# Performance work log

Hardware: AMD Instinct MI355X
Metric: run time of the kernel (lower is better)

## Reference

```python
import jax, jax.numpy as jnp
import numpy as np

N, E = 100000, 640000
IN_DIM, OUT_DIM, H, D = 128, 128, 4, 32  # head_dim = out_dim // num_heads
NUM_EDGE_TYPES = 3
NEG_SLOPE = 0.2


def setup_inputs() -> dict:
    key = jax.random.key(0)
    ks = jax.random.split(key, 10)
    x = jax.random.normal(ks[0], (N, IN_DIM), dtype=jnp.float32)
    edge_index = jax.random.randint(ks[1], (2, E), 0, N, dtype=jnp.int32)
    edge_type = jax.random.randint(ks[2], (E,), 0, NUM_EDGE_TYPES, dtype=jnp.int32)
    s = 1.0 / np.sqrt(IN_DIM)
    Wq = jax.random.uniform(ks[3], (IN_DIM, H * D), jnp.float32, -s, s)
    Wk = jax.random.uniform(ks[4], (IN_DIM, H * D), jnp.float32, -s, s)
    Wv = jax.random.uniform(ks[5], (IN_DIM, H * D), jnp.float32, -s, s)
    # xavier_uniform on (1, H, 2D): gain*sqrt(6/(fan_in+fan_out)) with fans (2D, H)
    a = np.sqrt(6.0 / (2 * D + H))
    attn_lin = jax.random.uniform(ks[6], (1, H, 2 * D), jnp.float32, -a, a)
    edge_embed_table = jax.random.normal(ks[7], (NUM_EDGE_TYPES, H * D), dtype=jnp.float32)
    so = 1.0 / np.sqrt(H * D)
    Wout = jax.random.uniform(ks[8], (H * D, OUT_DIM), jnp.float32, -so, so)
    bout = jax.random.uniform(ks[9], (OUT_DIM,), jnp.float32, -so, so)
    return {"x": x, "Wq": Wq, "Wk": Wk, "Wv": Wv, "attn_lin": attn_lin,
            "edge_embed_table": edge_embed_table, "Wout": Wout, "bout": bout,
            "edge_index": edge_index, "edge_type": edge_type}


def reference(x, Wq, Wk, Wv, attn_lin, edge_embed_table, Wout, bout, edge_index, edge_type):
    n = x.shape[0]
    src, dst = edge_index[0], edge_index[1]
    q = (x @ Wq).reshape(n, H, D)
    k = (x @ Wk).reshape(n, H, D)
    v = (x @ Wv).reshape(n, H, D)
    q_src = q[src]            # (E, H, D)
    k_dst = k[dst]            # (E, H, D)
    # (cat([q_src,k_dst]) * attn_lin).sum(-1) == q_src.a_q + k_dst.a_k
    a_q, a_k = attn_lin[0, :, :D], attn_lin[0, :, D:]      # (H, D) each
    scores = jnp.einsum('ehd,hd->eh', q_src, a_q) + jnp.einsum('ehd,hd->eh', k_dst, a_k)
    scores = jnp.where(scores >= 0, scores, NEG_SLOPE * scores)  # leaky_relu
    edge_embed = edge_embed_table[edge_type].reshape(-1, H, D)
    scores = scores + jnp.sum(q_src * edge_embed, axis=-1)       # (E, H)
    # segmented softmax over destination node (detached max, clamped at -100)
    m = jax.ops.segment_max(jax.lax.stop_gradient(scores), dst, num_segments=n)
    m = jnp.maximum(m, -100.0)
    ex = jnp.exp(scores - m[dst])
    denom = jax.ops.segment_sum(ex, dst, num_segments=n)
    alpha = ex / (denom[dst] + 1e-10)                            # (E, H)
    messages = alpha[:, :, None] * v[src]                        # (E, H, D)
    out = jax.ops.segment_sum(messages, dst, num_segments=n)     # (N, H, D)
    out = out.reshape(n, H * D)
    return out @ Wout + bout
```

## Files before the change

### kernel.cpp

```cpp
#include <hip/hip_runtime.h>
#include <hip/hip_bf16.h>

#define H_   4
#define D_   32
#define HD   128
#define IND  128
#define OUTD 128
#define NET  3
#define NEG  0.2f
#define CAP  2048

typedef short short8 __attribute__((ext_vector_type(8)));
typedef float f32x4  __attribute__((ext_vector_type(4)));

#define AS_GLOBAL(p) ((const __attribute__((address_space(1))) unsigned int*)(p))
#define AS_LDS(p)    ((__attribute__((address_space(3))) unsigned int*)(p))

__device__ __forceinline__ unsigned short f2bf(float f) {
  union { __hip_bfloat16 b; unsigned short u; } x;
  x.b = __float2bfloat16(f);
  return x.u;
}

__device__ __forceinline__ short8 pack_bf8(float4 lo, float4 hi) {
  union { short8 s; unsigned short u[8]; } r;
  r.u[0] = f2bf(lo.x); r.u[1] = f2bf(lo.y); r.u[2] = f2bf(lo.z); r.u[3] = f2bf(lo.w);
  r.u[4] = f2bf(hi.x); r.u[5] = f2bf(hi.y); r.u[6] = f2bf(hi.z); r.u[7] = f2bf(hi.w);
  return r.s;
}

#define BFLO(x) __uint_as_float((x) << 16)
#define BFHI(x) __uint_as_float((x) & 0xFFFF0000u)

__global__ void k0b_pack(const float* __restrict__ Wq, const float* __restrict__ Wk,
                         const float* __restrict__ attn, const float* __restrict__ ee,
                         const float* __restrict__ Wv, const float* __restrict__ Wout,
                         unsigned short* __restrict__ Wallt,
                         unsigned short* __restrict__ Woutt,
                         int* __restrict__ gbuck, int nbuck) {
  int b = blockIdx.x, i = threadIdx.x;
  if (b == 288) {
    for (int k = i; k < nbuck; k += 128) gbuck[k] = 0;
    return;
  }
  if (b < 160) {
    int c = b;
    float val = 0.f;
    if (c < 128) {
      val = Wv[i*HD + c];
    } else {
      int cc = c - 128;
      if (cc < 4) {
        int h = cc;
        for (int d = 0; d < D_; d++) val += Wq[i*HD + h*D_ + d] * attn[h*2*D_ + d];
      } else if (cc < 16) {
        int t2 = (cc - 4) >> 2, h = (cc - 4) & 3;
        for (int d = 0; d < D_; d++) val += Wq[i*HD + h*D_ + d] * ee[t2*HD + h*D_ + d];
      } else if (cc < 20) {
        int h = cc - 16;
        for (int d = 0; d < D_; d++) val += Wk[i*HD + h*D_ + d] * attn[h*2*D_ + D_ + d];
      }
    }
    Wallt[(c*128 + i) ^ ((c & 7) << 3)] = f2bf(val);
  } else {
    int c = b - 160;
    Woutt[(c*128 + i) ^ ((c & 7) << 3)] = f2bf(Wout[i*OUTD + c]);
  }
}

__global__ __launch_bounds__(256) void k1b(const float* __restrict__ x,
    const uint4* __restrict__ Wallt,
    unsigned short* __restrict__ vb, unsigned short* __restrict__ nqb,
    float* __restrict__ skb, int n, int nbb,
    const int* __restrict__ ei, const int* __restrict__ et,
    int* __restrict__ gbuck, unsigned int* __restrict__ ebuf,
    int E_, int nbuck, int per) {
  extern __shared__ char dlds[];
  int t = threadIdx.x;
  if (blockIdx.x < nbb) {
    int* cnt  = (int*)dlds;
    int* base = cnt + 1024;
    for (int i = t; i < nbuck; i += 256) cnt[i] = 0;
    __syncthreads();
    int bb = blockIdx.x;
    int e0 = bb * per;
    int e1 = min(e0 + per, E_);
    for (int e = e0 + t; e < e1; e += 256)
      atomicAdd(&cnt[ei[E_ + e] >> 7], 1);
    __syncthreads();
    for (int i = t; i < nbuck; i += 256) {
      int c = cnt[i];
      base[i] = c ? atomicAdd(&gbuck[i], c) : 0;
      cnt[i] = 0;
    }
    __syncthreads();
    for (int e = e0 + t; e < e1; e += 256) {
      int d = ei[E_ + e];
      int b = d >> 7;
      int pos = base[b] + atomicAdd(&cnt[b], 1);
      ebuf[(size_t)b * CAP + pos] =
          (unsigned)ei[e] | ((unsigned)et[e] << 17) | ((unsigned)(d & 127) << 19);
    }
    return;
  }
  uint4* ldsB = (uint4*)dlds;
  int wv = t >> 6, lane = t & 63;
  int l15 = lane & 15, l16 = lane >> 4;
  int base = (blockIdx.x - nbb) * 64;
  int arow = base + wv*16 + l15;
  int rr = min(arow, n - 1);
  const float* xr = &x[(size_t)rr*IND + l16*8];
  float4 lo[4], hi[4];
  #pragma unroll
  for (int kk = 0; kk < 4; kk++) {
    lo[kk] = *(const float4*)(xr + kk*32);
    hi[kk] = *(const float4*)(xr + kk*32 + 4);
  }
  #pragma unroll
  for (int i = 0; i < 10; i++) {
    const uint4* gp = Wallt + i*256 + wv*64 + lane;
    uint4* lp = ldsB + i*256 + wv*64;
    __builtin_amdgcn_global_load_lds(AS_GLOBAL(gp), AS_LDS(lp), 16, 0, 0);
  }
  short8 afr[4];
  #pragma unroll
  for (int kk = 0; kk < 4; kk++) afr[kk] = pack_bf8(lo[kk], hi[kk]);
  __syncthreads();
  f32x4 acc[10];
  #pragma unroll
  for (int nt = 0; nt < 10; nt++) acc[nt] = (f32x4){0.f, 0.f, 0.f, 0.f};
  #pragma unroll
  for (int nt = 0; nt < 10; nt++) {
    int bcol = nt*16 + l15;
    #pragma unroll
    for (int kk = 0; kk < 4; kk++) {
      int bytec = kk*64 + l16*16;
      short8 b = *(const short8*)((const char*)ldsB + ((bcol*256 + bytec) ^ ((bcol & 7) << 4)));
      acc[nt] = __builtin_amdgcn_mfma_f32_16x16x32_bf16(afr[kk], b, acc[nt], 0, 0, 0);
    }
  }
  int rowbase = base + wv*16 + l16*4;
  #pragma unroll
  for (int nt = 0; nt < 10; nt++) {
    int col = nt*16 + l15;
    #pragma unroll
    for (int r = 0; r < 4; r++) {
      int row = rowbase + r;
      if (row >= n) continue;
      float val = acc[nt][r];
      if (nt < 8)       vb[(size_t)row*HD + col] = f2bf(val);
      else if (nt == 8) nqb[((size_t)row << 4) + (col - 128)] = f2bf(val);
      else { int c = col - 144; if (c < 4) skb[(size_t)row*4 + c] = val; }
    }
  }
}

__global__ __launch_bounds__(256) void k_sort(const unsigned int* __restrict__ ebuf,
    const int* __restrict__ gbuck, int* __restrict__ offsets,
    int* __restrict__ elist, int n, int E_) {
  __shared__ int cnt[128], cur[128], sc[128], red[256];
  int b = blockIdx.x, t = threadIdx.x;
  int part = 0;
  for (int i = t; i < b; i += 256) part += gbuck[i];
  red[t] = part; __syncthreads();
  for (int off = 128; off > 0; off >>= 1) {
    if (t < off) red[t] += red[t + off];
    __syncthreads();
  }
  int bb = red[0];
  int m = gbuck[b];
  if (b == 0 && t == 0) offsets[n] = E_;
  if (t < 128) cnt[t] = 0;
  __syncthreads();
  const unsigned int* eb = ebuf + (size_t)b * CAP;
  for (int i = t; i < m; i += 256)
    atomicAdd(&cnt[(eb[i] >> 19) & 127], 1);
  __syncthreads();
  if (t < 128) sc[t] = cnt[t];
  __syncthreads();
  for (int off = 1; off < 128; off <<= 1) {
    int v = (t >= off && t < 128) ? sc[t - off] : 0;
    __syncthreads();
    if (t < 128) sc[t] += v;
    __syncthreads();
  }
  if (t < 128) {
    int excl = sc[t] - cnt[t];
    cur[t] = excl;
    int dst = b * 128 + t;
    if (dst < n) offsets[dst] = bb + excl;
  }
  __syncthreads();
  for (int i = t; i < m; i += 256) {
    unsigned int w = eb[i];
    int dl = (w >> 19) & 127;
    int p = bb + atomicAdd(&cur[dl], 1);
    elist[p] = (int)((w & 0x1FFFFu) | (((w >> 17) & 3u) << 20));
  }
}

__global__ __launch_bounds__(256) void k3_agg(
    const int* __restrict__ offsets, const int* __restrict__ elist,
    const unsigned short* __restrict__ nqb, const float* __restrict__ skb,
    const unsigned short* __restrict__ vb, unsigned short* __restrict__ aggb, int n) {
  int t = threadIdx.x;
  int g = t >> 4, s = t & 15;
  int dst = blockIdx.x * 16 + g;
  __shared__ float s_esc[16][17][4];
  __shared__ int s_src[16][17];
  if (dst >= n) return;
  int off0 = offsets[dst];
  int deg = offsets[dst + 1] - off0;
  int h = s >> 2;
  unsigned short* orow = &aggb[(size_t)dst*HD + s*8];
  if (deg == 0) {
    *(uint4*)orow = make_uint4(0u, 0u, 0u, 0u);
    return;
  }
  float4 sk4 = *(const float4*)(&skb[(size_t)dst*4]);
  float dp0 = 0.f, dp1 = 0.f, dp2 = 0.f, dp3 = 0.f;
  float a0=0.f,a1=0.f,a2=0.f,a3=0.f,a4=0.f,a5=0.f,a6=0.f,a7=0.f;
  for (int bas = 0; bas < deg; bas += 16) {
    int cnt = min(16, deg - bas);
    float e0 = 0.f, e1 = 0.f, e2 = 0.f, e3 = 0.f;
    int srcoff = 0;
    if (s < cnt) {
      int p = elist[off0 + bas + s];
      int src = p & 0xFFFFF;
      int ety = p >> 20;
      const unsigned short* nr = nqb + ((size_t)src << 4);
      uint2 sqp = *(const uint2*)nr;
      uint2 qep = *(const uint2*)(nr + 4 + ety*4);
      float s0 = BFLO(sqp.x) + sk4.x;
      float s1 = BFHI(sqp.x) + sk4.y;
      float s2 = BFLO(sqp.y) + sk4.z;
      float s3 = BFHI(sqp.y) + sk4.w;
      s0 = (s0 >= 0.f ? s0 : NEG*s0) + BFLO(qep.x); e0 = __expf(s0);
      s1 = (s1 >= 0.f ? s1 : NEG*s1) + BFHI(qep.x); e1 = __expf(s1);
      s2 = (s2 >= 0.f ? s2 : NEG*s2) + BFLO(qep.y); e2 = __expf(s2);
      s3 = (s3 >= 0.f ? s3 : NEG*s3) + BFHI(qep.y); e3 = __expf(s3);
      dp0 += e0; dp1 += e1; dp2 += e2; dp3 += e3;
      srcoff = src << 7;
    }
    s_src[g][s] = srcoff;
    *(float4*)(&s_esc[g][s][0]) = make_float4(e0, e1, e2, e3);
    __builtin_amdgcn_wave_barrier();
    int e = 0;
    for (; e + 4 <= cnt; e += 4) {
      float al0 = s_esc[g][e+0][h], al1 = s_esc[g][e+1][h];
      float al2 = s_esc[g][e+2][h], al3 = s_esc[g][e+3][h];
      const unsigned short* p0 = vb + s_src[g][e+0] + s*8;
      const unsigned short* p1 = vb + s_src[g][e+1] + s*8;
      const unsigned short* p2 = vb + s_src[g][e+2] + s*8;
      const unsigned short* p3 = vb + s_src[g][e+3] + s*8;
      uint4 v0 = *(const uint4*)p0;
      uint4 v1 = *(const uint4*)p1;
      uint4 v2 = *(const uint4*)p2;
      uint4 v3 = *(const uint4*)p3;
      a0 += al0 * BFLO(v0.x); a1 += al0 * BFHI(v0.x);
      a2 += al0 * BFLO(v0.y); a3 += al0 * BFHI(v0.y);
      a4 += al0 * BFLO(v0.z); a5 += al0 * BFHI(v0.z);
      a6 += al0 * BFLO(v0.w); a7 += al0 * BFHI(v0.w);
      a0 += al1 * BFLO(v1.x); a1 += al1 * BFHI(v1.x);
      a2 += al1 * BFLO(v1.y); a3 += al1 * BFHI(v1.y);
      a4 += al1 * BFLO(v1.z); a5 += al1 * BFHI(v1.z);
      a6 += al1 * BFLO(v1.w); a7 += al1 * BFHI(v1.w);
      a0 += al2 * BFLO(v2.x); a1 += al2 * BFHI(v2.x);
      a2 += al2 * BFLO(v2.y); a3 += al2 * BFHI(v2.y);
      a4 += al2 * BFLO(v2.z); a5 += al2 * BFHI(v2.z);
      a6 += al2 * BFLO(v2.w); a7 += al2 * BFHI(v2.w);
      a0 += al3 * BFLO(v3.x); a1 += al3 * BFHI(v3.x);
      a2 += al3 * BFLO(v3.y); a3 += al3 * BFHI(v3.y);
      a4 += al3 * BFLO(v3.z); a5 += al3 * BFHI(v3.z);
      a6 += al3 * BFLO(v3.w); a7 += al3 * BFHI(v3.w);
    }
    for (; e < cnt; e++) {
      float a = s_esc[g][e][h];
      const unsigned short* p = vb + s_src[g][e] + s*8;
      uint4 vv = *(const uint4*)p;
      a0 += a * BFLO(vv.x); a1 += a * BFHI(vv.x);
      a2 += a * BFLO(vv.y); a3 += a * BFHI(vv.y);
      a4 += a * BFLO(vv.z); a5 += a * BFHI(vv.z);
      a6 += a * BFLO(vv.w); a7 += a * BFHI(vv.w);
    }
    __builtin_amdgcn_wave_barrier();
  }
  #pragma unroll
  for (int off = 1; off < 16; off <<= 1) {
    dp0 += __shfl_xor(dp0, off);
    dp1 += __shfl_xor(dp1, off);
    dp2 += __shfl_xor(dp2, off);
    dp3 += __shfl_xor(dp3, off);
  }
  float den = (h == 0) ? dp0 : (h == 1) ? dp1 : (h == 2) ? dp2 : dp3;
  float inv = 1.f / (den + 1e-10f);
  uint4 pk;
  pk.x = (unsigned)f2bf(a0*inv) | ((unsigned)f2bf(a1*inv) << 16);
  pk.y = (unsigned)f2bf(a2*inv) | ((unsigned)f2bf(a3*inv) << 16);
  pk.z = (unsigned)f2bf(a4*inv) | ((unsigned)f2bf(a5*inv) << 16);
  pk.w = (unsigned)f2bf(a6*inv) | ((unsigned)f2bf(a7*inv) << 16);
  *(uint4*)orow = pk;
}

__global__ __launch_bounds__(256) void k4_gemm(const unsigned short* __restrict__ aggb,
    const uint4* __restrict__ Woutt, const float* __restrict__ bout,
    float* __restrict__ out, int n) {
  __shared__ uint4 ldsB[2048];
  int t = threadIdx.x;
  #pragma unroll
  for (int i = 0; i < 8; i++) ldsB[i*256 + t] = Woutt[i*256 + t];
  int wv = t >> 6, lane = t & 63;
  int l15 = lane & 15, l16 = lane >> 4;
  int base = blockIdx.x * 64;
  int arow = base + wv*16 + l15;
  int rr = min(arow, n - 1);
  const unsigned short* ar = &aggb[(size_t)rr*HD + l16*8];
  short8 afr[4];
  #pragma unroll
  for (int kk = 0; kk < 4; kk++)
    afr[kk] = *(const short8*)(ar + kk*32);
  __syncthreads();
  f32x4 acc[8];
  #pragma unroll
  for (int nt = 0; nt < 8; nt++) acc[nt] = (f32x4){0.f, 0.f, 0.f, 0.f};
  #pragma unroll
  for (int nt = 0; nt < 8; nt++) {
    int bcol = nt*16 + l15;
    #pragma unroll
    for (int kk = 0; kk < 4; kk++) {
      int bytec = kk*64 + l16*16;
      short8 b = *(const short8*)((const char*)ldsB + ((bcol*256 + bytec) ^ ((bcol & 7) << 4)));
      acc[nt] = __builtin_amdgcn_mfma_f32_16x16x32_bf16(afr[kk], b, acc[nt], 0, 0, 0);
    }
  }
  int rowbase = base + wv*16 + l16*4;
  #pragma unroll
  for (int nt = 0; nt < 8; nt++) {
    int col = nt*16 + l15;
    float bv = bout[col];
    #pragma unroll
    for (int r = 0; r < 4; r++) {
      int row = rowbase + r;
      if (row < n) out[(size_t)row*OUTD + col] = acc[nt][r] + bv;
    }
  }
}

extern "C" void kernel_launch(void* const* d_in, const int* in_sizes, int n_in,
                              void* d_out, int out_size, void* d_ws, size_t ws_size,
                              hipStream_t stream) {
  const float* x    = (const float*)d_in[0];
  const float* Wq   = (const float*)d_in[1];
  const float* Wk   = (const float*)d_in[2];
  const float* Wv   = (const float*)d_in[3];
  const float* attn = (const float*)d_in[4];
  const float* ee   = (const float*)d_in[5];
  const float* Wout = (const float*)d_in[6];
  const float* bout = (const float*)d_in[7];
  const int*   ei   = (const int*)d_in[8];
  const int*   et   = (const int*)d_in[9];
  int n  = in_sizes[0] / IND;
  int E_ = in_sizes[9];
  float* out = (float*)d_out;
  int nbuck = (n + 127) >> 7;

  char* w = (char*)d_ws;
  auto alloc = [&](size_t bytes) {
    char* p = w;
    w += (bytes + 255) & ~(size_t)255;
    return p;
  };
  unsigned short* vb    = (unsigned short*)alloc((size_t)n * HD * 2);
  unsigned short* aggb  = (unsigned short*)alloc((size_t)n * HD * 2);
  unsigned short* nqb   = (unsigned short*)alloc((size_t)n * 16 * 2);
  float* skb      = (float*)alloc((size_t)n * 4 * 4);
  unsigned short* Wallt = (unsigned short*)alloc(160 * 128 * 2);
  unsigned short* Woutt = (unsigned short*)alloc(128 * 128 * 2);
  unsigned int* ebuf = (unsigned int*)alloc((size_t)nbuck * CAP * 4);
  int*   gbuck    = (int*)alloc((size_t)nbuck * 4);
  int*   offsets  = (int*)alloc(((size_t)n + 1) * 4);
  int*   elist    = (int*)alloc((size_t)E_ * 4);

  k0b_pack<<<289, 128, 0, stream>>>(Wq, Wk, attn, ee, Wv, Wout, Wallt, Woutt,
                                    gbuck, nbuck);
  int nblk1 = (n + 63) / 64;
  int nbb = 256;
  int per = (E_ + nbb - 1) / nbb;
  k1b<<<nbb + nblk1, 256, 40960, stream>>>(x, (const uint4*)Wallt, vb, nqb, skb,
                                           n, nbb, ei, et, gbuck, ebuf,
                                           E_, nbuck, per);
  k_sort<<<nbuck, 256, 0, stream>>>(ebuf, gbuck, offsets, elist, n, E_);
  k3_agg<<<(n + 15)/16, 256, 0, stream>>>(offsets, elist, nqb, skb, vb, aggb, n);
  k4_gemm<<<(n + 63)/64, 256, 0, stream>>>(aggb, (const uint4*)Woutt, bout, out, n);
}
```

Before: 98.18 us.

## Fuse per-bucket counting sort into aggregation kernel using LDS edge lists

Merges the bucket sort and the attention aggregation into one kernel. Each block sorts its 128-destination bucket into shared memory and then aggregates those destinations directly. This removes the global offsets/elist round trip, the prefix sum over buckets, and one launch. In exchange there are far fewer blocks (one per 128 nodes, about 782), each wave handles 8 destinations serially, and each block uses about 8KB+ of LDS, which may lower occupancy and latency hiding for the gather-heavy loop.

```diff
diff --git a/kernel.cpp b/kernel.cpp
--- a/kernel.cpp
+++ b/kernel.cpp
@@ -119,7 +119,7 @@
   #pragma unroll
   for (int i = 0; i < 10; i++) {
     const uint4* gp = Wallt + i*256 + wv*64 + lane;
-    uint4* lp = ldsB + i*256 + wv*64;
+    uint4* lp = (uint4*)dlds + i*256 + wv*64;
     __builtin_amdgcn_global_load_lds(AS_GLOBAL(gp), AS_LDS(lp), 16, 0, 0);
   }
   short8 afr[4];
@@ -155,21 +155,16 @@
   }
 }
 
-__global__ __launch_bounds__(256) void k_sort(const unsigned int* __restrict__ ebuf,
-    const int* __restrict__ gbuck, int* __restrict__ offsets,
-    int* __restrict__ elist, int n, int E_) {
-  __shared__ int cnt[128], cur[128], sc[128], red[256];
+__global__ __launch_bounds__(256) void k3f(const unsigned int* __restrict__ ebuf,
+    const int* __restrict__ gbuck,
+    const unsigned short* __restrict__ nqb, const float* __restrict__ skb,
+    const unsigned short* __restrict__ vb, unsigned short* __restrict__ aggb, int n) {
+  __shared__ unsigned int el[CAP];
+  __shared__ int cnt[128], cur[128], sc[128];
+  __shared__ float s_esc[16][17][4];
+  __shared__ int s_src[16][17];
   int b = blockIdx.x, t = threadIdx.x;
-  int part = 0;
-  for (int i = t; i < b; i += 256) part += gbuck[i];
-  red[t] = part; __syncthreads();
-  for (int off = 128; off > 0; off >>= 1) {
-    if (t < off) red[t] += red[t + off];
-    __syncthreads();
-  }
-  int bb = red[0];
   int m = gbuck[b];
-  if (b == 0 && t == 0) offsets[n] = E_;
   if (t < 128) cnt[t] = 0;
   __syncthreads();
   const unsigned int* eb = ebuf + (size_t)b * CAP;
@@ -184,122 +179,111 @@
     if (t < 128) sc[t] += v;
     __syncthreads();
   }
-  if (t < 128) {
-    int excl = sc[t] - cnt[t];
-    cur[t] = excl;
-    int dst = b * 128 + t;
-    if (dst < n) offsets[dst] = bb + excl;
-  }
+  if (t < 128) cur[t] = sc[t] - cnt[t];
   __syncthreads();
   for (int i = t; i < m; i += 256) {
     unsigned int w = eb[i];
     int dl = (w >> 19) & 127;
-    int p = bb + atomicAdd(&cur[dl], 1);
-    elist[p] = (int)((w & 0x1FFFFu) | (((w >> 17) & 3u) << 20));
-  }
-}
-
-__global__ __launch_bounds__(256) void k3_agg(
-    const int* __restrict__ offsets, const int* __restrict__ elist,
-    const unsigned short* __restrict__ nqb, const float* __restrict__ skb,
-    const unsigned short* __restrict__ vb, unsigned short* __restrict__ aggb, int n) {
-  int t = threadIdx.x;
+    el[atomicAdd(&cur[dl], 1)] = w;
+  }
+  __syncthreads();
   int g = t >> 4, s = t & 15;
-  int dst = blockIdx.x * 16 + g;
-  __shared__ float s_esc[16][17][4];
-  __shared__ int s_src[16][17];
-  if (dst >= n) return;
-  int off0 = offsets[dst];
-  int deg = offsets[dst + 1] - off0;
   int h = s >> 2;
-  unsigned short* orow = &aggb[(size_t)dst*HD + s*8];
-  if (deg == 0) {
-    *(uint4*)orow = make_uint4(0u, 0u, 0u, 0u);
-    return;
-  }
-  float4 sk4 = *(const float4*)(&skb[(size_t)dst*4]);
-  float dp0 = 0.f, dp1 = 0.f, dp2 = 0.f, dp3 = 0.f;
-  float a0=0.f,a1=0.f,a2=0.f,a3=0.f,a4=0.f,a5=0.f,a6=0.f,a7=0.f;
-  for (int bas = 0; bas < deg; bas += 16) {
-    int cnt = min(16, deg - bas);
-    float e0 = 0.f, e1 = 0.f, e2 = 0.f, e3 = 0.f;
-    int srcoff = 0;
-    if (s < cnt) {
-      int p = elist[off0 + bas + s];
-      int src = p & 0xFFFFF;
-      int ety = p >> 20;
-      const unsigned short* nr = nqb + ((size_t)src << 4);
-      uint2 sqp = *(const uint2*)nr;
-      uint2 qep = *(const uint2*)(nr + 4 + ety*4);
-      float s0 = BFLO(sqp.x) + sk4.x;
-      float s1 = BFHI(sqp.x) + sk4.y;
-      float s2 = BFLO(sqp.y) + sk4.z;
-      float s3 = BFHI(sqp.y) + sk4.w;
-      s0 = (s0 >= 0.f ? s0 : NEG*s0) + BFLO(qep.x); e0 = __expf(s0);
-      s1 = (s1 >= 0.f ? s1 : NEG*s1) + BFHI(qep.x); e1 = __expf(s1);
-      s2 = (s2 >= 0.f ? s2 : NEG*s2) + BFLO(qep.y); e2 = __expf(s2);
-      s3 = (s3 >= 0.f ? s3 : NEG*s3) + BFHI(qep.y); e3 = __expf(s3);
-      dp0 += e0; dp1 += e1; dp2 += e2; dp3 += e3;
-      srcoff = src << 7;
-    }
-    s_src[g][s] = srcoff;
-    *(float4*)(&s_esc[g][s][0]) = make_float4(e0, e1, e2, e3);
-    __builtin_amdgcn_wave_barrier();
-    int e = 0;
-    for (; e + 4 <= cnt; e += 4) {
-      float al0 = s_esc[g][e+0][h], al1 = s_esc[g][e+1][h];
-      float al2 = s_esc[g][e+2][h], al3 = s_esc[g][e+3][h];
-      const unsigned short* p0 = vb + s_src[g][e+0] + s*8;
-      const unsigned short* p1 = vb + s_src[g][e+1] + s*8;
-      const unsigned short* p2 = vb + s_src[g][e+2] + s*8;
-      const unsigned short* p3 = vb + s_src[g][e+3] + s*8;
-      uint4 v0 = *(const uint4*)p0;
-      uint4 v1 = *(const uint4*)p1;
-      uint4 v2 = *(const uint4*)p2;
-      uint4 v3 = *(const uint4*)p3;
-      a0 += al0 * BFLO(v0.x); a1 += al0 * BFHI(v0.x);
-      a2 += al0 * BFLO(v0.y); a3 += al0 * BFHI(v0.y);
-      a4 += al0 * BFLO(v0.z); a5 += al0 * BFHI(v0.z);
-      a6 += al0 * BFLO(v0.w); a7 += al0 * BFHI(v0.w);
-      a0 += al1 * BFLO(v1.x); a1 += al1 * BFHI(v1.x);
-      a2 += al1 * BFLO(v1.y); a3 += al1 * BFHI(v1.y);
-      a4 += al1 * BFLO(v1.z); a5 += al1 * BFHI(v1.z);
-      a6 += al1 * BFLO(v1.w); a7 += al1 * BFHI(v1.w);
-      a0 += al2 * BFLO(v2.x); a1 += al2 * BFHI(v2.x);
-      a2 += al2 * BFLO(v2.y); a3 += al2 * BFHI(v2.y);
-      a4 += al2 * BFLO(v2.z); a5 += al2 * BFHI(v2.z);
-      a6 += al2 * BFLO(v2.w); a7 += al2 * BFHI(v2.w);
-      a0 += al3 * BFLO(v3.x); a1 += al3 * BFHI(v3.x);
-      a2 += al3 * BFLO(v3.y); a3 += al3 * BFHI(v3.y);
-      a4 += al3 * BFLO(v3.z); a5 += al3 * BFHI(v3.z);
-      a6 += al3 * BFLO(v3.w); a7 += al3 * BFHI(v3.w);
-    }
-    for (; e < cnt; e++) {
-      float a = s_esc[g][e][h];
-      const unsigned short* p = vb + s_src[g][e] + s*8;
-      uint4 vv = *(const uint4*)p;
-      a0 += a * BFLO(vv.x); a1 += a * BFHI(vv.x);
-      a2 += a * BFLO(vv.y); a3 += a * BFHI(vv.y);
-      a4 += a * BFLO(vv.z); a5 += a * BFHI(vv.z);
-      a6 += a * BFLO(vv.w); a7 += a * BFHI(vv.w);
-    }
-    __builtin_amdgcn_wave_barrier();
-  }
-  #pragma unroll
-  for (int off = 1; off < 16; off <<= 1) {
-    dp0 += __shfl_xor(dp0, off);
-    dp1 += __shfl_xor(dp1, off);
-    dp2 += __shfl_xor(dp2, off);
-    dp3 += __shfl_xor(dp3, off);
-  }
-  float den = (h == 0) ? dp0 : (h == 1) ? dp1 : (h == 2) ? dp2 : dp3;
-  float inv = 1.f / (den + 1e-10f);
-  uint4 pk;
-  pk.x = (unsigned)f2bf(a0*inv) | ((unsigned)f2bf(a1*inv) << 16);
-  pk.y = (unsigned)f2bf(a2*inv) | ((unsigned)f2bf(a3*inv) << 16);
-  pk.z = (unsigned)f2bf(a4*inv) | ((unsigned)f2bf(a5*inv) << 16);
-  pk.w = (unsigned)f2bf(a6*inv) | ((unsigned)f2bf(a7*inv) << 16);
-  *(uint4*)orow = pk;
+  for (int k = 0; k < 8; k++) {
+    int dl = g*8 + k;
+    int dst = b*128 + dl;
+    if (dst >= n) continue;
+    int deg = cnt[dl];
+    unsigned short* orow = &aggb[(size_t)dst*HD + s*8];
+    if (deg == 0) {
+      *(uint4*)orow = make_uint4(0u, 0u, 0u, 0u);
+      continue;
+    }
+    int off0 = sc[dl] - deg;
+    float4 sk4 = *(const float4*)(&skb[(size_t)dst*4]);
+    float dp0 = 0.f, dp1 = 0.f, dp2 = 0.f, dp3 = 0.f;
+    float a0=0.f,a1=0.f,a2=0.f,a3=0.f,a4=0.f,a5=0.f,a6=0.f,a7=0.f;
+    for (int bas = 0; bas < deg; bas += 16) {
+      int cnt2 = min(16, deg - bas);
+      float e0 = 0.f, e1 = 0.f, e2 = 0.f, e3 = 0.f;
+      int srcoff = 0;
+      if (s < cnt2) {
+        unsigned int p = el[off0 + bas + s];
+        int src = p & 0x1FFFF;
+        int ety = (p >> 17) & 3;
+        const unsigned short* nr = nqb + ((size_t)src << 4);
+        uint2 sqp = *(const uint2*)nr;
+        uint2 qep = *(const uint2*)(nr + 4 + ety*4);
+        float s0 = BFLO(sqp.x) + sk4.x;
+        float s1 = BFHI(sqp.x) + sk4.y;
+        float s2 = BFLO(sqp.y) + sk4.z;
+        float s3 = BFHI(sqp.y) + sk4.w;
+        s0 = (s0 >= 0.f ? s0 : NEG*s0) + BFLO(qep.x); e0 = __expf(s0);
+        s1 = (s1 >= 0.f ? s1 : NEG*s1) + BFHI(qep.x); e1 = __expf(s1);
+        s2 = (s2 >= 0.f ? s2 : NEG*s2) + BFLO(qep.y); e2 = __expf(s2);
+        s3 = (s3 >= 0.f ? s3 : NEG*s3) + BFHI(qep.y); e3 = __expf(s3);
+        dp0 += e0; dp1 += e1; dp2 += e2; dp3 += e3;
+        srcoff = src << 7;
+      }
+      s_src[g][s] = srcoff;
+      *(float4*)(&s_esc[g][s][0]) = make_float4(e0, e1, e2, e3);
+      __builtin_amdgcn_wave_barrier();
+      int e = 0;
+      for (; e + 4 <= cnt2; e += 4) {
+        float al0 = s_esc[g][e+0][h], al1 = s_esc[g][e+1][h];
+        float al2 = s_esc[g][e+2][h], al3 = s_esc[g][e+3][h];
+        const unsigned short* p0 = vb + s_src[g][e+0] + s*8;
+        const unsigned short* p1 = vb + s_src[g][e+1] + s*8;
+        const unsigned short* p2 = vb + s_src[g][e+2] + s*8;
+        const unsigned short* p3 = vb + s_src[g][e+3] + s*8;
+        uint4 v0 = *(const uint4*)p0;
+        uint4 v1 = *(const uint4*)p1;
+        uint4 v2 = *(const uint4*)p2;
+        uint4 v3 = *(const uint4*)p3;
+        a0 += al0 * BFLO(v0.x); a1 += al0 * BFHI(v0.x);
+        a2 += al0 * BFLO(v0.y); a3 += al0 * BFHI(v0.y);
+        a4 += al0 * BFLO(v0.z); a5 += al0 * BFHI(v0.z);
+        a6 += al0 * BFLO(v0.w); a7 += al0 * BFHI(v0.w);
+        a0 += al1 * BFLO(v1.x); a1 += al1 * BFHI(v1.x);
+        a2 += al1 * BFLO(v1.y); a3 += al1 * BFHI(v1.y);
+        a4 += al1 * BFLO(v1.z); a5 += al1 * BFHI(v1.z);
+        a6 += al1 * BFLO(v1.w); a7 += al1 * BFHI(v1.w);
+        a0 += al2 * BFLO(v2.x); a1 += al2 * BFHI(v2.x);
+        a2 += al2 * BFLO(v2.y); a3 += al2 * BFHI(v2.y);
+        a4 += al2 * BFLO(v2.z); a5 += al2 * BFHI(v2.z);
+        a6 += al2 * BFLO(v2.w); a7 += al2 * BFHI(v2.w);
+        a0 += al3 * BFLO(v3.x); a1 += al3 * BFHI(v3.x);
+        a2 += al3 * BFLO(v3.y); a3 += al3 * BFHI(v3.y);
+        a4 += al3 * BFLO(v3.z); a5 += al3 * BFHI(v3.z);
+        a6 += al3 * BFLO(v3.w); a7 += al3 * BFHI(v3.w);
+      }
+      for (; e < cnt2; e++) {
+        float a = s_esc[g][e][h];
+        const unsigned short* p = vb + s_src[g][e] + s*8;
+        uint4 vv = *(const uint4*)p;
+        a0 += a * BFLO(vv.x); a1 += a * BFHI(vv.x);
+        a2 += a * BFLO(vv.y); a3 += a * BFHI(vv.y);
+        a4 += a * BFLO(vv.z); a5 += a * BFHI(vv.z);
+        a6 += a * BFLO(vv.w); a7 += a * BFHI(vv.w);
+      }
+      __builtin_amdgcn_wave_barrier();
+    }
+    #pragma unroll
+    for (int off = 1; off < 16; off <<= 1) {
+      dp0 += __shfl_xor(dp0, off);
+      dp1 += __shfl_xor(dp1, off);
+      dp2 += __shfl_xor(dp2, off);
+      dp3 += __shfl_xor(dp3, off);
+    }
+    float den = (h == 0) ? dp0 : (h == 1) ? dp1 : (h == 2) ? dp2 : dp3;
+    float inv = 1.f / (den + 1e-10f);
+    uint4 pk;
+    pk.x = (unsigned)f2bf(a0*inv) | ((unsigned)f2bf(a1*inv) << 16);
+    pk.y = (unsigned)f2bf(a2*inv) | ((unsigned)f2bf(a3*inv) << 16);
+    pk.z = (unsigned)f2bf(a4*inv) | ((unsigned)f2bf(a5*inv) << 16);
+    pk.w = (unsigned)f2bf(a6*inv) | ((unsigned)f2bf(a7*inv) << 16);
+    *(uint4*)orow = pk;
+  }
 }
 
 __global__ __launch_bounds__(256) void k4_gemm(const unsigned short* __restrict__ aggb,
@@ -378,8 +362,6 @@
   unsigned short* Woutt = (unsigned short*)alloc(128 * 128 * 2);
   unsigned int* ebuf = (unsigned int*)alloc((size_t)nbuck * CAP * 4);
   int*   gbuck    = (int*)alloc((size_t)nbuck * 4);
-  int*   offsets  = (int*)alloc(((size_t)n + 1) * 4);
-  int*   elist    = (int*)alloc((size_t)E_ * 4);
 
   k0b_pack<<<289, 128, 0, stream>>>(Wq, Wk, attn, ee, Wv, Wout, Wallt, Woutt,
                                     gbuck, nbuck);
@@ -389,7 +371,6 @@
   k1b<<<nbb + nblk1, 256, 40960, stream>>>(x, (const uint4*)Wallt, vb, nqb, skb,
                                            n, nbb, ei, et, gbuck, ebuf,
                                            E_, nbuck, per);
-  k_sort<<<nbuck, 256, 0, stream>>>(ebuf, gbuck, offsets, elist, n, E_);
-  k3_agg<<<(n + 15)/16, 256, 0, stream>>>(offsets, elist, nqb, skb, vb, aggb, n);
+  k3f<<<nbuck, 256, 0, stream>>>(ebuf, gbuck, nqb, skb, vb, aggb, n);
   k4_gemm<<<(n + 63)/64, 256, 0, stream>>>(aggb, (const uint4*)Woutt, bout, out, n);
 }
```

After: 98.81 us. Within noise of the previous version (+0.6%).
